# Kernel tuning notes

Measured on AMD Instinct MI355X. Metric: run time of the kernel, lower is better.

## Reference

```python
import jax, jax.numpy as jnp
import numpy as np

B, N, DIM = 4, 16384, 512
HEADS, DHEAD = 8, 64
INNER = HEADS * DHEAD  # 512
ID_NUM = 128           # window size
EPS = 1e-5


def _ln(x, g, b):
    m = jnp.mean(x, axis=-1, keepdims=True)
    v = jnp.mean(jnp.square(x - m), axis=-1, keepdims=True)
    return (x - m) * jax.lax.rsqrt(v + EPS) * g + b


def setup_inputs() -> dict:
    key = jax.random.key(0)
    ks = jax.random.split(key, 10)
    s_in = 1.0 / np.sqrt(DIM)
    s_inner = 1.0 / np.sqrt(INNER)
    return {
        "x": jax.random.normal(ks[0], (B, N, DIM), jnp.float32),
        "y": jax.random.normal(ks[1], (B, N, DIM), jnp.float32),
        # torch Linear weights are [out, in]
        "Wq": jax.random.normal(ks[2], (INNER, DIM), jnp.float32) * s_in,
        "gq": jnp.ones((INNER,), jnp.float32),
        "bq": jnp.zeros((INNER,), jnp.float32),
        "Wk": jax.random.normal(ks[3], (INNER, DIM), jnp.float32) * s_in,
        "gk": jnp.ones((INNER,), jnp.float32),
        "bk": jnp.zeros((INNER,), jnp.float32),
        "Wv": jax.random.normal(ks[4], (INNER, DIM), jnp.float32) * s_in,
        "Wout": jax.random.normal(ks[5], (DIM, INNER), jnp.float32) * s_inner,
        "bout": jnp.zeros((DIM,), jnp.float32),
    }


def reference(x, y, Wq, gq, bq, Wk, gk, bk, Wv, Wout, bout):
    b, n, _ = y.shape
    w = n // ID_NUM
    scale = DHEAD ** -0.5

    q = _ln(y @ Wq.T, gq, bq)   # [b, n, inner]
    k = _ln(x @ Wk.T, gk, bk)
    v = x @ Wv.T

    # 'b (w n) (h d) -> (b w) h n d'
    def split(t):
        return t.reshape(b * w, ID_NUM, HEADS, DHEAD).transpose(0, 2, 1, 3)

    q, k, v = split(q), split(k), split(v)
    dots = jnp.einsum('bhid,bhjd->bhij', q, k) * scale  # [(b w), h, id, id]
    attn = jax.nn.softmax(dots, axis=-1)
    out = jnp.einsum('bhij,bhjd->bhid', attn, v)
    # '(b w) h n d -> b (w n) (h d)'
    out = out.transpose(0, 2, 1, 3).reshape(b, n, INNER)
    y_new = y + out @ Wout.T + bout
    return (y_new, attn)
```

## Files before the change

### kernel.cpp

```cpp
#include <hip/hip_runtime.h>


typedef __attribute__((ext_vector_type(8))) short short8;
typedef __attribute__((ext_vector_type(4))) float f32x4;
typedef __attribute__((ext_vector_type(4))) unsigned short us4;
typedef __attribute__((ext_vector_type(8))) unsigned short us8;
typedef __attribute__((ext_vector_type(4))) float fv4;

__device__ __forceinline__ unsigned short f2bf(float f) {
  unsigned u = __builtin_bit_cast(unsigned, f);
  u += 0x7fffu + ((u >> 16) & 1u);
  return (unsigned short)(u >> 16);
}
__device__ __forceinline__ float bf2f(unsigned short h) {
  unsigned u = ((unsigned)h) << 16;
  return __builtin_bit_cast(float, u);
}

__global__ __launch_bounds__(256) void cvt_kernel(const float* __restrict__ src,
                                                  unsigned short* __restrict__ dst,
                                                  int n4) {
  int i = blockIdx.x * 256 + threadIdx.x;
  if (i >= n4) return;
  fv4 f = *(const fv4*)(src + (size_t)i * 4);
  us4 o;
  o[0] = f2bf(f[0]); o[1] = f2bf(f[1]); o[2] = f2bf(f[2]); o[3] = f2bf(f[3]);
  *(us4*)(dst + (size_t)i * 4) = o;
}

template <int FINAL>
__global__ __launch_bounds__(256) void gemm_bt(const unsigned short* __restrict__ A,
                                               const unsigned short* __restrict__ Bw,
                                               unsigned short* __restrict__ Cb,
                                               float* __restrict__ Cf,
                                               const float* __restrict__ yres,
                                               const float* __restrict__ bias) {
  __shared__ __align__(16) unsigned short As[128 * 32];
  __shared__ __align__(16) unsigned short Bs[128 * 32];
  const int tid = threadIdx.x;
  const int lane = tid & 63;
  const int wv = tid >> 6;
  const int quad = lane >> 4;
  const int l16 = lane & 15;
  const size_t m0 = (size_t)blockIdx.x * 128;
  const int n0 = blockIdx.y * 128;
  const int wm = (wv >> 1) * 64;
  const int wn = (wv & 1) * 64;

  f32x4 acc[4][4];
#pragma unroll
  for (int i = 0; i < 4; i++)
#pragma unroll
    for (int j = 0; j < 4; j++) acc[i][j] = (f32x4){0.f, 0.f, 0.f, 0.f};

  int ma[2], koff[2];
#pragma unroll
  for (int i = 0; i < 2; i++) {
    int c = i * 256 + tid;
    int m = c >> 2;
    int kc = (c & 3) ^ ((m >> 2) & 3);
    ma[i] = m;
    koff[i] = kc * 16;
  }
  const char* Ab = (const char*)A;
  const char* Bb = (const char*)Bw;
  char* AsB = (char*)As;
  char* BsB = (char*)Bs;

  for (int ks = 0; ks < 512; ks += 32) {
#pragma unroll
    for (int i = 0; i < 2; i++) {
      const char* ga = Ab + ((m0 + (size_t)ma[i]) << 10) + ks * 2 + koff[i];
      const char* gb = Bb + (((size_t)(n0 + ma[i])) << 10) + ks * 2 + koff[i];
      __builtin_amdgcn_global_load_lds(
          (const __attribute__((address_space(1))) unsigned int*)ga,
          (__attribute__((address_space(3))) unsigned int*)(AsB + i * 4096 + wv * 1024),
          16, 0, 0);
      __builtin_amdgcn_global_load_lds(
          (const __attribute__((address_space(1))) unsigned int*)gb,
          (__attribute__((address_space(3))) unsigned int*)(BsB + i * 4096 + wv * 1024),
          16, 0, 0);
    }
    __syncthreads();

    short8 af[4], bf[4];
#pragma unroll
    for (int t = 0; t < 4; t++) {
      int m = wm + t * 16 + l16;
      af[t] = *(const short8*)&As[m * 32 + ((quad ^ ((m >> 2) & 3)) * 8)];
      int n = wn + t * 16 + l16;
      bf[t] = *(const short8*)&Bs[n * 32 + ((quad ^ ((n >> 2) & 3)) * 8)];
    }
#pragma unroll
    for (int mt = 0; mt < 4; mt++)
#pragma unroll
      for (int nt = 0; nt < 4; nt++)
        acc[mt][nt] =
            __builtin_amdgcn_mfma_f32_16x16x32_bf16(af[mt], bf[nt], acc[mt][nt], 0, 0, 0);
    __syncthreads();
  }

#pragma unroll
  for (int mt = 0; mt < 4; mt++) {
    size_t mrow = m0 + wm + mt * 16 + quad * 4;
#pragma unroll
    for (int nt = 0; nt < 4; nt++) {
      int n = n0 + wn + nt * 16 + l16;
#pragma unroll
      for (int r = 0; r < 4; r++) {
        size_t idx = (mrow + r) * 512 + n;
        if (FINAL) {
          Cf[idx] = acc[mt][nt][r] + yres[idx] + bias[n];
        } else {
          Cb[idx] = f2bf(acc[mt][nt][r]);
        }
      }
    }
  }
}

__global__ __launch_bounds__(256) void ln_rows(unsigned short* __restrict__ t,
                                               const float* __restrict__ g,
                                               const float* __restrict__ b) {
  size_t row = (size_t)blockIdx.x * 4 + (threadIdx.x >> 6);
  int lane = threadIdx.x & 63;
  unsigned short* p = t + row * 512 + lane * 8;
  us8 raw = *(const us8*)p;
  float v[8];
#pragma unroll
  for (int i = 0; i < 8; i++) v[i] = bf2f(raw[i]);
  float s = 0.f;
#pragma unroll
  for (int i = 0; i < 8; i++) s += v[i];
#pragma unroll
  for (int off = 32; off; off >>= 1) s += __shfl_xor(s, off);
  float mean = s * (1.0f / 512.0f);
  float qs = 0.f;
#pragma unroll
  for (int i = 0; i < 8; i++) {
    float d = v[i] - mean;
    qs += d * d;
  }
#pragma unroll
  for (int off = 32; off; off >>= 1) qs += __shfl_xor(qs, off);
  float rstd = rsqrtf(qs * (1.0f / 512.0f) + 1e-5f);
  const float* gp = g + lane * 8;
  const float* bp = b + lane * 8;
  us8 o;
#pragma unroll
  for (int i = 0; i < 8; i++) o[i] = f2bf((v[i] - mean) * rstd * gp[i] + bp[i]);
  *(us8*)p = o;
}

__global__ __launch_bounds__(256) void attn_kernel(const unsigned short* __restrict__ q,
                                                   const unsigned short* __restrict__ kmat,
                                                   const unsigned short* __restrict__ v,
                                                   float* __restrict__ attn_out,
                                                   unsigned short* __restrict__ ctx) {
  __shared__ __align__(16) unsigned short vT[64 * 128];
  __shared__ __align__(16) unsigned short Ps[128 * 128];
  const int h = blockIdx.x;
  const int bw = blockIdx.y;
  const int tb = bw * 128;
  const int tid = threadIdx.x;
  const int lane = tid & 63;
  const int wv = tid >> 6;
  const int quad = lane >> 4;
  const int l16 = lane & 15;
  const int hoff = h * 64;

#pragma unroll
  for (int it = 0; it < 8; it++) {
    int idx = (it * 256 + tid) * 4;
    int t = idx >> 6;
    int d = idx & 63;
    us4 val = *(const us4*)&v[(size_t)(tb + t) * 512 + hoff + d];
#pragma unroll
    for (int j = 0; j < 4; j++) {
      int dd = d + j;
      int cp = (t >> 3) ^ (dd & 15);
      vT[dd * 128 + cp * 8 + (t & 7)] = val[j];
    }
  }

  f32x4 acc[2][8];
#pragma unroll
  for (int mi = 0; mi < 2; mi++)
#pragma unroll
    for (int ni = 0; ni < 8; ni++) acc[mi][ni] = (f32x4){0.f, 0.f, 0.f, 0.f};

  short8 aq[2][2];
#pragma unroll
  for (int mi = 0; mi < 2; mi++) {
    int tok = tb + wv * 32 + mi * 16 + l16;
#pragma unroll
    for (int kk = 0; kk < 2; kk++)
      aq[mi][kk] = *(const short8*)&q[(size_t)tok * 512 + hoff + kk * 32 + quad * 8];
  }
#pragma unroll
  for (int ni = 0; ni < 8; ni++) {
    int ktok = tb + ni * 16 + l16;
    short8 bk0 = *(const short8*)&kmat[(size_t)ktok * 512 + hoff + quad * 8];
    short8 bk1 = *(const short8*)&kmat[(size_t)ktok * 512 + hoff + 32 + quad * 8];
#pragma unroll
    for (int mi = 0; mi < 2; mi++) {
      acc[mi][ni] = __builtin_amdgcn_mfma_f32_16x16x32_bf16(aq[mi][0], bk0, acc[mi][ni], 0, 0, 0);
      acc[mi][ni] = __builtin_amdgcn_mfma_f32_16x16x32_bf16(aq[mi][1], bk1, acc[mi][ni], 0, 0, 0);
    }
  }

  const float c1 = 0.125f * 1.44269504088896f;
  size_t abase = ((size_t)(bw * 8 + h)) << 14;
#pragma unroll
  for (int mi = 0; mi < 2; mi++) {
#pragma unroll
    for (int r = 0; r < 4; r++) {
      float mx = acc[mi][0][r];
#pragma unroll
      for (int ni = 1; ni < 8; ni++) mx = fmaxf(mx, acc[mi][ni][r]);
      mx = fmaxf(mx, __shfl_xor(mx, 1));
      mx = fmaxf(mx, __shfl_xor(mx, 2));
      mx = fmaxf(mx, __shfl_xor(mx, 4));
      mx = fmaxf(mx, __shfl_xor(mx, 8));
      float pv[8];
      float sum = 0.f;
#pragma unroll
      for (int ni = 0; ni < 8; ni++) {
        pv[ni] = __expf((acc[mi][ni][r] - mx) * 0.125f);
        sum += pv[ni];
      }
      sum += __shfl_xor(sum, 1);
      sum += __shfl_xor(sum, 2);
      sum += __shfl_xor(sum, 4);
      sum += __shfl_xor(sum, 8);
      float inv = 1.0f / sum;
      int i = wv * 32 + mi * 16 + quad * 4 + r;
#pragma unroll
      for (int ni = 0; ni < 8; ni++) {
        float p = pv[ni] * inv;
        int j = ni * 16 + l16;
        attn_out[abase + (size_t)i * 128 + j] = p;
        int cp = (j >> 3) ^ (i & 15);
        Ps[i * 128 + cp * 8 + (j & 7)] = f2bf(p);
      }
    }
  }
  (void)c1;
  __syncthreads();

  f32x4 o[2][4];
#pragma unroll
  for (int mi = 0; mi < 2; mi++)
#pragma unroll
    for (int nt = 0; nt < 4; nt++) o[mi][nt] = (f32x4){0.f, 0.f, 0.f, 0.f};

#pragma unroll
  for (int ks = 0; ks < 4; ks++) {
    short8 bfr[4];
#pragma unroll
    for (int nt = 0; nt < 4; nt++) {
      int d = nt * 16 + l16;
      int cp = (ks * 4 + quad) ^ (d & 15);
      bfr[nt] = *(const short8*)&vT[d * 128 + cp * 8];
    }
#pragma unroll
    for (int mi = 0; mi < 2; mi++) {
      int i = wv * 32 + mi * 16 + l16;
      int cp = (ks * 4 + quad) ^ (i & 15);
      short8 afr = *(const short8*)&Ps[i * 128 + cp * 8];
#pragma unroll
      for (int nt = 0; nt < 4; nt++)
        o[mi][nt] = __builtin_amdgcn_mfma_f32_16x16x32_bf16(afr, bfr[nt], o[mi][nt], 0, 0, 0);
    }
  }
#pragma unroll
  for (int mi = 0; mi < 2; mi++)
#pragma unroll
    for (int nt = 0; nt < 4; nt++)
#pragma unroll
      for (int r = 0; r < 4; r++) {
        int tok = tb + wv * 32 + mi * 16 + quad * 4 + r;
        int d = nt * 16 + l16;
        ctx[(size_t)tok * 512 + hoff + d] = f2bf(o[mi][nt][r]);
      }
}

extern "C" void kernel_launch(void* const* d_in, const int* in_sizes, int n_in,
                              void* d_out, int out_size, void* d_ws, size_t ws_size,
                              hipStream_t stream) {
  const float* x = (const float*)d_in[0];
  const float* y = (const float*)d_in[1];
  const float* Wq = (const float*)d_in[2];
  const float* gq = (const float*)d_in[3];
  const float* bq = (const float*)d_in[4];
  const float* Wk = (const float*)d_in[5];
  const float* gk = (const float*)d_in[6];
  const float* bk = (const float*)d_in[7];
  const float* Wv = (const float*)d_in[8];
  const float* Wout = (const float*)d_in[9];
  const float* bout = (const float*)d_in[10];
  float* out = (float*)d_out;

  char* ws = (char*)d_ws;
  const size_t W = 524288;
  const size_t T = 67108864;
  unsigned short* WQB = (unsigned short*)(ws);
  unsigned short* WKB = (unsigned short*)(ws + W);
  unsigned short* WVB = (unsigned short*)(ws + 2 * W);
  unsigned short* WOB = (unsigned short*)(ws + 3 * W);
  unsigned short* XB = (unsigned short*)(ws + 4 * W);
  unsigned short* YB = (unsigned short*)(ws + 4 * W + T);
  unsigned short* Q = (unsigned short*)(ws + 4 * W + 2 * T);
  unsigned short* Kb = (unsigned short*)(ws + 4 * W + 3 * T);
  unsigned short* Vb = (unsigned short*)(ws + 4 * W + 4 * T);
  unsigned short* CTX = YB;

  cvt_kernel<<<256, 256, 0, stream>>>(Wq, WQB, 65536);
  cvt_kernel<<<256, 256, 0, stream>>>(Wk, WKB, 65536);
  cvt_kernel<<<256, 256, 0, stream>>>(Wv, WVB, 65536);
  cvt_kernel<<<256, 256, 0, stream>>>(Wout, WOB, 65536);
  cvt_kernel<<<32768, 256, 0, stream>>>(x, XB, 8388608);
  cvt_kernel<<<32768, 256, 0, stream>>>(y, YB, 8388608);

  dim3 gg(512, 4);
  gemm_bt<0><<<gg, 256, 0, stream>>>(YB, WQB, Q, nullptr, nullptr, nullptr);
  gemm_bt<0><<<gg, 256, 0, stream>>>(XB, WKB, Kb, nullptr, nullptr, nullptr);
  gemm_bt<0><<<gg, 256, 0, stream>>>(XB, WVB, Vb, nullptr, nullptr, nullptr);

  ln_rows<<<16384, 256, 0, stream>>>(Q, gq, bq);
  ln_rows<<<16384, 256, 0, stream>>>(Kb, gk, bk);

  attn_kernel<<<dim3(8, 512), 256, 0, stream>>>(Q, Kb, Vb, out + 33554432, CTX);

  gemm_bt<1><<<gg, 256, 0, stream>>>(CTX, WOB, nullptr, out, y, bout);
}
```

Baseline: 1.018 ms.

## Swap MFMA operands for vectorized epilogue stores and fuse K/V projection GEMM

The MFMA A/B operands are swapped so each lane holds four consecutive columns of the output. That lets the GEMM epilogue, the softmax probability writes (attention matrix and the LDS P tile) and the context output use 4-wide vector stores instead of scalar strided ones. Softmax row reductions now shuffle across quads instead of within 16 lanes. The K and V projections are merged into one GEMM over concatenated weights with leading dimension 1024, so X is read once. The cost is a strided KV layout and a more complex indexing scheme.

```diff
diff --git a/kernel.cpp b/kernel.cpp
--- a/kernel.cpp
+++ b/kernel.cpp
@@ -34,7 +34,8 @@
                                                unsigned short* __restrict__ Cb,
                                                float* __restrict__ Cf,
                                                const float* __restrict__ yres,
-                                               const float* __restrict__ bias) {
+                                               const float* __restrict__ bias,
+                                               int ldc) {
   __shared__ __align__(16) unsigned short As[128 * 32];
   __shared__ __align__(16) unsigned short Bs[128 * 32];
   const int tid = threadIdx.x;
@@ -96,24 +97,29 @@
 #pragma unroll
       for (int nt = 0; nt < 4; nt++)
         acc[mt][nt] =
-            __builtin_amdgcn_mfma_f32_16x16x32_bf16(af[mt], bf[nt], acc[mt][nt], 0, 0, 0);
+            __builtin_amdgcn_mfma_f32_16x16x32_bf16(bf[nt], af[mt], acc[mt][nt], 0, 0, 0);
     __syncthreads();
   }
 
 #pragma unroll
   for (int mt = 0; mt < 4; mt++) {
-    size_t mrow = m0 + wm + mt * 16 + quad * 4;
+    size_t m = m0 + wm + mt * 16 + l16;
 #pragma unroll
     for (int nt = 0; nt < 4; nt++) {
-      int n = n0 + wn + nt * 16 + l16;
-#pragma unroll
-      for (int r = 0; r < 4; r++) {
-        size_t idx = (mrow + r) * 512 + n;
-        if (FINAL) {
-          Cf[idx] = acc[mt][nt][r] + yres[idx] + bias[n];
-        } else {
-          Cb[idx] = f2bf(acc[mt][nt][r]);
-        }
+      int n = n0 + wn + nt * 16 + quad * 4;
+      size_t idx = m * (size_t)ldc + n;
+      if (FINAL) {
+        fv4 yv = *(const fv4*)(yres + idx);
+        fv4 bv = *(const fv4*)(bias + n);
+        fv4 o;
+#pragma unroll
+        for (int r = 0; r < 4; r++) o[r] = acc[mt][nt][r] + yv[r] + bv[r];
+        *(fv4*)(Cf + idx) = o;
+      } else {
+        us4 o;
+#pragma unroll
+        for (int r = 0; r < 4; r++) o[r] = f2bf(acc[mt][nt][r]);
+        *(us4*)(Cb + idx) = o;
       }
     }
   }
@@ -121,10 +127,11 @@
 
 __global__ __launch_bounds__(256) void ln_rows(unsigned short* __restrict__ t,
                                                const float* __restrict__ g,
-                                               const float* __restrict__ b) {
+                                               const float* __restrict__ b,
+                                               int ld) {
   size_t row = (size_t)blockIdx.x * 4 + (threadIdx.x >> 6);
   int lane = threadIdx.x & 63;
-  unsigned short* p = t + row * 512 + lane * 8;
+  unsigned short* p = t + row * (size_t)ld + lane * 8;
   us8 raw = *(const us8*)p;
   float v[8];
 #pragma unroll
@@ -151,6 +158,8 @@
   for (int i = 0; i < 8; i++) o[i] = f2bf((v[i] - mean) * rstd * gp[i] + bp[i]);
   *(us8*)p = o;
 }
+
+#define KVLD 1024
 
 __global__ __launch_bounds__(256) void attn_kernel(const unsigned short* __restrict__ q,
                                                    const unsigned short* __restrict__ kmat,
@@ -174,7 +183,7 @@
     int idx = (it * 256 + tid) * 4;
     int t = idx >> 6;
     int d = idx & 63;
-    us4 val = *(const us4*)&v[(size_t)(tb + t) * 512 + hoff + d];
+    us4 val = *(const us4*)&v[(size_t)(tb + t) * KVLD + hoff + d];
 #pragma unroll
     for (int j = 0; j < 4; j++) {
       int dd = d + j;
@@ -200,52 +209,55 @@
 #pragma unroll
   for (int ni = 0; ni < 8; ni++) {
     int ktok = tb + ni * 16 + l16;
-    short8 bk0 = *(const short8*)&kmat[(size_t)ktok * 512 + hoff + quad * 8];
-    short8 bk1 = *(const short8*)&kmat[(size_t)ktok * 512 + hoff + 32 + quad * 8];
+    short8 bk0 = *(const short8*)&kmat[(size_t)ktok * KVLD + hoff + quad * 8];
+    short8 bk1 = *(const short8*)&kmat[(size_t)ktok * KVLD + hoff + 32 + quad * 8];
 #pragma unroll
     for (int mi = 0; mi < 2; mi++) {
-      acc[mi][ni] = __builtin_amdgcn_mfma_f32_16x16x32_bf16(aq[mi][0], bk0, acc[mi][ni], 0, 0, 0);
-      acc[mi][ni] = __builtin_amdgcn_mfma_f32_16x16x32_bf16(aq[mi][1], bk1, acc[mi][ni], 0, 0, 0);
-    }
-  }
-
-  const float c1 = 0.125f * 1.44269504088896f;
+      acc[mi][ni] = __builtin_amdgcn_mfma_f32_16x16x32_bf16(bk0, aq[mi][0], acc[mi][ni], 0, 0, 0);
+      acc[mi][ni] = __builtin_amdgcn_mfma_f32_16x16x32_bf16(bk1, aq[mi][1], acc[mi][ni], 0, 0, 0);
+    }
+  }
+
   size_t abase = ((size_t)(bw * 8 + h)) << 14;
 #pragma unroll
   for (int mi = 0; mi < 2; mi++) {
-#pragma unroll
-    for (int r = 0; r < 4; r++) {
-      float mx = acc[mi][0][r];
-#pragma unroll
-      for (int ni = 1; ni < 8; ni++) mx = fmaxf(mx, acc[mi][ni][r]);
-      mx = fmaxf(mx, __shfl_xor(mx, 1));
-      mx = fmaxf(mx, __shfl_xor(mx, 2));
-      mx = fmaxf(mx, __shfl_xor(mx, 4));
-      mx = fmaxf(mx, __shfl_xor(mx, 8));
-      float pv[8];
-      float sum = 0.f;
-#pragma unroll
-      for (int ni = 0; ni < 8; ni++) {
-        pv[ni] = __expf((acc[mi][ni][r] - mx) * 0.125f);
-        sum += pv[ni];
+    float mx = acc[mi][0][0];
+#pragma unroll
+    for (int ni = 0; ni < 8; ni++)
+#pragma unroll
+      for (int r = 0; r < 4; r++) mx = fmaxf(mx, acc[mi][ni][r]);
+    mx = fmaxf(mx, __shfl_xor(mx, 16));
+    mx = fmaxf(mx, __shfl_xor(mx, 32));
+    float pv[8][4];
+    float sum = 0.f;
+#pragma unroll
+    for (int ni = 0; ni < 8; ni++)
+#pragma unroll
+      for (int r = 0; r < 4; r++) {
+        pv[ni][r] = __expf((acc[mi][ni][r] - mx) * 0.125f);
+        sum += pv[ni][r];
       }
-      sum += __shfl_xor(sum, 1);
-      sum += __shfl_xor(sum, 2);
-      sum += __shfl_xor(sum, 4);
-      sum += __shfl_xor(sum, 8);
-      float inv = 1.0f / sum;
-      int i = wv * 32 + mi * 16 + quad * 4 + r;
-#pragma unroll
-      for (int ni = 0; ni < 8; ni++) {
-        float p = pv[ni] * inv;
-        int j = ni * 16 + l16;
-        attn_out[abase + (size_t)i * 128 + j] = p;
-        int cp = (j >> 3) ^ (i & 15);
-        Ps[i * 128 + cp * 8 + (j & 7)] = f2bf(p);
+    sum += __shfl_xor(sum, 16);
+    sum += __shfl_xor(sum, 32);
+    float inv = 1.0f / sum;
+    int i = wv * 32 + mi * 16 + l16;
+    int cpx = (i & 15);
+#pragma unroll
+    for (int ni = 0; ni < 8; ni++) {
+      int j0 = ni * 16 + quad * 4;
+      fv4 pq;
+      us4 pb;
+#pragma unroll
+      for (int r = 0; r < 4; r++) {
+        float p = pv[ni][r] * inv;
+        pq[r] = p;
+        pb[r] = f2bf(p);
       }
-    }
-  }
-  (void)c1;
+      *(fv4*)&attn_out[abase + (size_t)i * 128 + j0] = pq;
+      int cp = (j0 >> 3) ^ cpx;
+      *(us4*)&Ps[i * 128 + cp * 8 + (quad & 1) * 4] = pb;
+    }
+  }
   __syncthreads();
 
   f32x4 o[2][4];
@@ -256,33 +268,35 @@
 
 #pragma unroll
   for (int ks = 0; ks < 4; ks++) {
-    short8 bfr[4];
+    short8 vfr[4];
 #pragma unroll
     for (int nt = 0; nt < 4; nt++) {
       int d = nt * 16 + l16;
       int cp = (ks * 4 + quad) ^ (d & 15);
-      bfr[nt] = *(const short8*)&vT[d * 128 + cp * 8];
+      vfr[nt] = *(const short8*)&vT[d * 128 + cp * 8];
     }
 #pragma unroll
     for (int mi = 0; mi < 2; mi++) {
       int i = wv * 32 + mi * 16 + l16;
       int cp = (ks * 4 + quad) ^ (i & 15);
-      short8 afr = *(const short8*)&Ps[i * 128 + cp * 8];
+      short8 pfr = *(const short8*)&Ps[i * 128 + cp * 8];
 #pragma unroll
       for (int nt = 0; nt < 4; nt++)
-        o[mi][nt] = __builtin_amdgcn_mfma_f32_16x16x32_bf16(afr, bfr[nt], o[mi][nt], 0, 0, 0);
-    }
-  }
-#pragma unroll
-  for (int mi = 0; mi < 2; mi++)
-#pragma unroll
-    for (int nt = 0; nt < 4; nt++)
-#pragma unroll
-      for (int r = 0; r < 4; r++) {
-        int tok = tb + wv * 32 + mi * 16 + quad * 4 + r;
-        int d = nt * 16 + l16;
-        ctx[(size_t)tok * 512 + hoff + d] = f2bf(o[mi][nt][r]);
-      }
+        o[mi][nt] = __builtin_amdgcn_mfma_f32_16x16x32_bf16(vfr[nt], pfr, o[mi][nt], 0, 0, 0);
+    }
+  }
+#pragma unroll
+  for (int mi = 0; mi < 2; mi++) {
+    int tok = tb + wv * 32 + mi * 16 + l16;
+#pragma unroll
+    for (int nt = 0; nt < 4; nt++) {
+      int d0 = nt * 16 + quad * 4;
+      us4 ov;
+#pragma unroll
+      for (int r = 0; r < 4; r++) ov[r] = f2bf(o[mi][nt][r]);
+      *(us4*)&ctx[(size_t)tok * 512 + hoff + d0] = ov;
+    }
+  }
 }
 
 extern "C" void kernel_launch(void* const* d_in, const int* in_sizes, int n_in,
@@ -305,32 +319,28 @@
   const size_t W = 524288;
   const size_t T = 67108864;
   unsigned short* WQB = (unsigned short*)(ws);
-  unsigned short* WKB = (unsigned short*)(ws + W);
-  unsigned short* WVB = (unsigned short*)(ws + 2 * W);
+  unsigned short* WKVB = (unsigned short*)(ws + W);
   unsigned short* WOB = (unsigned short*)(ws + 3 * W);
   unsigned short* XB = (unsigned short*)(ws + 4 * W);
   unsigned short* YB = (unsigned short*)(ws + 4 * W + T);
   unsigned short* Q = (unsigned short*)(ws + 4 * W + 2 * T);
-  unsigned short* Kb = (unsigned short*)(ws + 4 * W + 3 * T);
-  unsigned short* Vb = (unsigned short*)(ws + 4 * W + 4 * T);
+  unsigned short* KV = (unsigned short*)(ws + 4 * W + 3 * T);
   unsigned short* CTX = YB;
 
   cvt_kernel<<<256, 256, 0, stream>>>(Wq, WQB, 65536);
-  cvt_kernel<<<256, 256, 0, stream>>>(Wk, WKB, 65536);
-  cvt_kernel<<<256, 256, 0, stream>>>(Wv, WVB, 65536);
+  cvt_kernel<<<256, 256, 0, stream>>>(Wk, WKVB, 65536);
+  cvt_kernel<<<256, 256, 0, stream>>>(Wv, WKVB + 262144, 65536);
   cvt_kernel<<<256, 256, 0, stream>>>(Wout, WOB, 65536);
   cvt_kernel<<<32768, 256, 0, stream>>>(x, XB, 8388608);
   cvt_kernel<<<32768, 256, 0, stream>>>(y, YB, 8388608);
 
-  dim3 gg(512, 4);
-  gemm_bt<0><<<gg, 256, 0, stream>>>(YB, WQB, Q, nullptr, nullptr, nullptr);
-  gemm_bt<0><<<gg, 256, 0, stream>>>(XB, WKB, Kb, nullptr, nullptr, nullptr);
-  gemm_bt<0><<<gg, 256, 0, stream>>>(XB, WVB, Vb, nullptr, nullptr, nullptr);
-
-  ln_rows<<<16384, 256, 0, stream>>>(Q, gq, bq);
-  ln_rows<<<16384, 256, 0, stream>>>(Kb, gk, bk);
-
-  attn_kernel<<<dim3(8, 512), 256, 0, stream>>>(Q, Kb, Vb, out + 33554432, CTX);
-
-  gemm_bt<1><<<gg, 256, 0, stream>>>(CTX, WOB, nullptr, out, y, bout);
-}
+  gemm_bt<0><<<dim3(512, 4), 256, 0, stream>>>(YB, WQB, Q, nullptr, nullptr, nullptr, 512);
+  gemm_bt<0><<<dim3(512, 8), 256, 0, stream>>>(XB, WKVB, KV, nullptr, nullptr, nullptr, 1024);
+
+  ln_rows<<<16384, 256, 0, stream>>>(Q, gq, bq, 512);
+  ln_rows<<<16384, 256, 0, stream>>>(KV, gk, bk, 1024);
+
+  attn_kernel<<<dim3(8, 512), 256, 0, stream>>>(Q, KV, KV + 512, out + 33554432, CTX);
+
+  gemm_bt<1><<<dim3(512, 4), 256, 0, stream>>>(CTX, WOB, nullptr, out, y, bout, 512);
+}
```

Measured after the change: 1.023 ms. Within noise of the previous version (+0.5%).
